# Optimization experiments

Measured on AMD Instinct MI355X. Metric: run time of the kernel, lower is better.

The kernel has to match this reference:

```python
import jax, jax.numpy as jnp
import numpy as np

N_NODES = 100000
N_EDGES = 1600000
D = 64


def setup_inputs() -> dict:
    key = jax.random.key(0)
    ks = jax.random.split(key, 9)
    x = jax.random.normal(ks[0], (N_NODES, D), dtype=jnp.float32)
    src = jax.random.randint(ks[1], (N_EDGES,), 0, N_NODES, dtype=jnp.int64)
    dst = jax.random.randint(ks[2], (N_EDGES,), 0, N_NODES, dtype=jnp.int64)
    s = 1.0 / np.sqrt(D)
    W_self1 = jax.random.normal(ks[3], (D, D), dtype=jnp.float32) * s
    W_neigh1 = jax.random.normal(ks[4], (D, D), dtype=jnp.float32) * s
    b1 = jnp.zeros((D,), dtype=jnp.float32)
    W_self2 = jax.random.normal(ks[5], (D, D), dtype=jnp.float32) * s
    W_neigh2 = jax.random.normal(ks[6], (D, D), dtype=jnp.float32) * s
    b2 = jnp.zeros((D,), dtype=jnp.float32)
    return {"x": x, "src": src, "dst": dst,
            "W_self1": W_self1, "W_neigh1": W_neigh1, "b1": b1,
            "W_self2": W_self2, "W_neigh2": W_neigh2, "b2": b2}


def _sage_layer(h, src, dst, W_self, W_neigh, b, n_nodes):
    # gather source-node features along edges: [E, d]
    msg = h[src]
    # sum messages into destination nodes, then normalize by in-degree (mean agg)
    agg = jax.ops.segment_sum(msg, dst, num_segments=n_nodes)
    deg = jax.ops.segment_sum(jnp.ones((src.shape[0], 1), h.dtype), dst,
                              num_segments=n_nodes)
    h_neigh = agg / jnp.maximum(deg, 1.0)
    # DGL SAGEConv (mean): fc_self(h) + fc_neigh(h_neigh) + bias
    return h @ W_self + h_neigh @ W_neigh + b


def reference(x, src, dst, W_self1, W_neigh1, b1, W_self2, W_neigh2, b2):
    n = x.shape[0]
    h = _sage_layer(x, src, dst, W_self1, W_neigh1, b1, n)
    # note: source module's forward applies no activation between layers
    h = _sage_layer(h, src, dst, W_self2, W_neigh2, b2, n)
    return h
```

## Files before the change

### kernel.cpp

```cpp
#include <hip/hip_runtime.h>
#include <hip/hip_bf16.h>


#define D 64
#define CAP 64
#define BNODES 256
#define BCAP 4736
#define MAXNB 512

typedef __bf16 bf16x8 __attribute__((ext_vector_type(8)));
typedef float  f32x4  __attribute__((ext_vector_type(4)));

__device__ __forceinline__ unsigned pack2(float a, float b) {
    __hip_bfloat162 t = __float22bfloat162_rn(make_float2(a, b));
    return *(unsigned*)&t;
}
__device__ __forceinline__ unsigned short f2b(float f) {
    __hip_bfloat16 b = __float2bfloat16(f);
    return *(unsigned short*)&b;
}


__global__ void __launch_bounds__(256)
cvt_kernel(const float4* __restrict__ x, uint4* __restrict__ y, int n8) {
    int i = blockIdx.x * blockDim.x + threadIdx.x;
    if (i < n8) {
        float4 a = x[2 * i], b = x[2 * i + 1];
        uint4 o;
        o.x = pack2(a.x, a.y);
        o.y = pack2(a.z, a.w);
        o.z = pack2(b.x, b.y);
        o.w = pack2(b.z, b.w);
        y[i] = o;
    }
}


__global__ void __launch_bounds__(64)
zrow_kernel(unsigned* __restrict__ a, unsigned* __restrict__ b) {
    int t = threadIdx.x;
    if (t < 32) a[t] = 0u;
    else        b[t - 32] = 0u;
}


__global__ void __launch_bounds__(256)
bin_kernel(const int* __restrict__ src, const int* __restrict__ dst,
           int* __restrict__ gcur, int* __restrict__ gbucket, int E, int NB) {
    __shared__ int hist[MAXNB];
    for (int i = threadIdx.x; i < NB; i += 256) hist[i] = 0;
    __syncthreads();

    const int t        = threadIdx.x;
    const int e4_total = E >> 2;
    const int base4    = blockIdx.x * 1024;

    int4 sv[4], dv[4];
    bool have[4];
    #pragma unroll
    for (int k = 0; k < 4; ++k) {
        int i4 = base4 + t + k * 256;
        have[k] = i4 < e4_total;
        if (have[k]) {
            sv[k] = ((const int4*)src)[i4];
            dv[k] = ((const int4*)dst)[i4];
        }
    }

    #pragma unroll
    for (int k = 0; k < 4; ++k) if (have[k]) {
        atomicAdd(&hist[dv[k].x >> 8], 1);
        atomicAdd(&hist[dv[k].y >> 8], 1);
        atomicAdd(&hist[dv[k].z >> 8], 1);
        atomicAdd(&hist[dv[k].w >> 8], 1);
    }

    int  tail_s = 0, tail_d = 0;
    bool have_tail = false;
    if (blockIdx.x == 0) {
        int e = (e4_total << 2) + t;
        if (e < E) {
            tail_s = src[e]; tail_d = dst[e]; have_tail = true;
            atomicAdd(&hist[tail_d >> 8], 1);
        }
    }
    __syncthreads();

    for (int i = threadIdx.x; i < NB; i += 256) {
        int c = hist[i];
        hist[i] = (c > 0) ? atomicAdd(&gcur[i], c) : 0;
    }
    __syncthreads();

    #pragma unroll
    for (int k = 0; k < 4; ++k) if (have[k]) {
        int4 s = sv[k], d = dv[k];
        int b, p;
        b = d.x >> 8; p = atomicAdd(&hist[b], 1); if (p < BCAP) gbucket[b * BCAP + p] = ((d.x & 255) << 17) | s.x;
        b = d.y >> 8; p = atomicAdd(&hist[b], 1); if (p < BCAP) gbucket[b * BCAP + p] = ((d.y & 255) << 17) | s.y;
        b = d.z >> 8; p = atomicAdd(&hist[b], 1); if (p < BCAP) gbucket[b * BCAP + p] = ((d.z & 255) << 17) | s.z;
        b = d.w >> 8; p = atomicAdd(&hist[b], 1); if (p < BCAP) gbucket[b * BCAP + p] = ((d.w & 255) << 17) | s.w;
    }
    if (have_tail) {
        int b = tail_d >> 8, p = atomicAdd(&hist[b], 1);
        if (p < BCAP) gbucket[b * BCAP + p] = ((tail_d & 255) << 17) | tail_s;
    }
}


__global__ void __launch_bounds__(256)
ellify_kernel(const int* __restrict__ gcur, const int* __restrict__ gbucket,
              int* __restrict__ cnt, int* __restrict__ edge_idx, int N) {
    __shared__ int scnt[BNODES];
    scnt[threadIdx.x] = 0;
    __syncthreads();

    const int b     = blockIdx.x;
    const int ne    = min(gcur[b], BCAP);
    const int node0 = b << 8;

    for (int e = threadIdx.x; e < ne; e += 256) {
        int p   = gbucket[b * BCAP + e];
        int s   = p & 0x1FFFF;
        int ld  = p >> 17;
        int pos = atomicAdd(&scnt[ld], 1);
        if (pos < CAP) edge_idx[(size_t)(node0 + ld) * CAP + pos] = s;
    }
    __syncthreads();

    int node = node0 + threadIdx.x;
    if (node < N) {
        int raw = scnt[threadIdx.x];
        cnt[node] = raw;
        int c  = min(raw, CAP);
        int c8 = (c + 7) & ~7;
        for (int p = c; p < c8; ++p)
            edge_idx[(size_t)node * CAP + p] = N;
    }
}


__device__ __forceinline__ void acc8(float& a0, float& a1, float& a2, float& a3,
                                     float& a4, float& a5, float& a6, float& a7,
                                     uint4 u) {
    a0 += __uint_as_float(u.x << 16);
    a1 += __uint_as_float(u.x & 0xffff0000u);
    a2 += __uint_as_float(u.y << 16);
    a3 += __uint_as_float(u.y & 0xffff0000u);
    a4 += __uint_as_float(u.z << 16);
    a5 += __uint_as_float(u.z & 0xffff0000u);
    a6 += __uint_as_float(u.w << 16);
    a7 += __uint_as_float(u.w & 0xffff0000u);
}

__global__ void __launch_bounds__(256, 4)
gather_kernel(const unsigned short* __restrict__ h,
              const int* __restrict__ cnt,
              const int* __restrict__ edge_idx,
              unsigned short* __restrict__ agg, int N) {
    const int lane = threadIdx.x & 63;
    const int q    = lane & 7;
    const int g    = lane >> 3;
    const int wave = blockIdx.x * (blockDim.x >> 6) + (threadIdx.x >> 6);
    const int node = wave * 8 + g;
    if (node >= N) return;

    const uint4* __restrict__ h4 = (const uint4*)h;

    const int count = min(cnt[node], CAP);
    const int c8    = (count + 7) & ~7;
    const int start = node * CAP;

    float a0 = 0.f, a1 = 0.f, a2 = 0.f, a3 = 0.f;
    float a4 = 0.f, a5 = 0.f, a6 = 0.f, a7 = 0.f;

    for (int j = 0; j < c8; j += 8) {
        const int sreg = edge_idx[start + j + q];
        const int b0 = g << 3;
        const int s0 = __shfl(sreg, b0 + 0, 64);
        const int s1 = __shfl(sreg, b0 + 1, 64);
        const int s2 = __shfl(sreg, b0 + 2, 64);
        const int s3 = __shfl(sreg, b0 + 3, 64);
        const int s4 = __shfl(sreg, b0 + 4, 64);
        const int s5 = __shfl(sreg, b0 + 5, 64);
        const int s6 = __shfl(sreg, b0 + 6, 64);
        const int s7 = __shfl(sreg, b0 + 7, 64);
        uint4 u0 = h4[(size_t)s0 * 8 + q];
        uint4 u1 = h4[(size_t)s1 * 8 + q];
        uint4 u2 = h4[(size_t)s2 * 8 + q];
        uint4 u3 = h4[(size_t)s3 * 8 + q];
        uint4 u4 = h4[(size_t)s4 * 8 + q];
        uint4 u5 = h4[(size_t)s5 * 8 + q];
        uint4 u6 = h4[(size_t)s6 * 8 + q];
        uint4 u7 = h4[(size_t)s7 * 8 + q];
        acc8(a0, a1, a2, a3, a4, a5, a6, a7, u0);
        acc8(a0, a1, a2, a3, a4, a5, a6, a7, u1);
        acc8(a0, a1, a2, a3, a4, a5, a6, a7, u2);
        acc8(a0, a1, a2, a3, a4, a5, a6, a7, u3);
        acc8(a0, a1, a2, a3, a4, a5, a6, a7, u4);
        acc8(a0, a1, a2, a3, a4, a5, a6, a7, u5);
        acc8(a0, a1, a2, a3, a4, a5, a6, a7, u6);
        acc8(a0, a1, a2, a3, a4, a5, a6, a7, u7);
    }

    const float inv = 1.0f / fmaxf((float)count, 1.0f);
    uint4 o;
    o.x = pack2(a0 * inv, a1 * inv);
    o.y = pack2(a2 * inv, a3 * inv);
    o.z = pack2(a4 * inv, a5 * inv);
    o.w = pack2(a6 * inv, a7 * inv);
    ((uint4*)agg)[node * 8 + q] = o;
}


__device__ __forceinline__ bf16x8 cvt8(float4 a, float4 b) {
    union { bf16x8 v; __hip_bfloat162 p[4]; } u;
    u.p[0] = __float22bfloat162_rn(make_float2(a.x, a.y));
    u.p[1] = __float22bfloat162_rn(make_float2(a.z, a.w));
    u.p[2] = __float22bfloat162_rn(make_float2(b.x, b.y));
    u.p[3] = __float22bfloat162_rn(make_float2(b.z, b.w));
    return u.v;
}
__device__ __forceinline__ bf16x8 asbf(uint4 u) {
    union { uint4 a; bf16x8 v; } c; c.a = u; return c.v;
}

__global__ void __launch_bounds__(256)
combine_kernel(const unsigned short* __restrict__ h,
               const unsigned short* __restrict__ agg,
               const float* __restrict__ Wself,
               const float* __restrict__ Wneigh,
               const float* __restrict__ bias,
               float* __restrict__ out_f32,
               unsigned short* __restrict__ out_bf16, int N) {
    const int lane = threadIdx.x & 63;
    const int col  = lane & 15;
    const int quad = lane >> 4;
    const int wave = blockIdx.x * (blockDim.x >> 6) + (threadIdx.x >> 6);
    const int n_waves = gridDim.x * (blockDim.x >> 6);

    bf16x8 Bf[4][4];
    #pragma unroll
    for (int nt = 0; nt < 4; ++nt) {
        const int n = nt * 16 + col;
        #pragma unroll
        for (int kk = 0; kk < 4; ++kk) {
            const float* W = (kk < 2) ? Wself : Wneigh;
            const int kbase = (kk & 1) * 32 + quad * 8;
            float w0 = W[(kbase + 0) * D + n];
            float w1 = W[(kbase + 1) * D + n];
            float w2 = W[(kbase + 2) * D + n];
            float w3 = W[(kbase + 3) * D + n];
            float w4 = W[(kbase + 4) * D + n];
            float w5 = W[(kbase + 5) * D + n];
            float w6 = W[(kbase + 6) * D + n];
            float w7 = W[(kbase + 7) * D + n];
            Bf[nt][kk] = cvt8(make_float4(w0, w1, w2, w3), make_float4(w4, w5, w6, w7));
        }
    }

    float bv[4];
    #pragma unroll
    for (int nt = 0; nt < 4; ++nt) bv[nt] = bias[nt * 16 + col];

    const uint4* __restrict__ h4 = (const uint4*)h;
    const uint4* __restrict__ a4 = (const uint4*)agg;

    const int tiles = (N + 15) >> 4;
    for (int t = wave; t < tiles; t += n_waves) {
        int row = t * 16 + col;
        if (row >= N) row = N - 1;

        bf16x8 A0 = asbf(h4[(size_t)row * 8 + quad]);
        bf16x8 A1 = asbf(h4[(size_t)row * 8 + 4 + quad]);
        bf16x8 A2 = asbf(a4[(size_t)row * 8 + quad]);
        bf16x8 A3 = asbf(a4[(size_t)row * 8 + 4 + quad]);

        #pragma unroll
        for (int nt = 0; nt < 4; ++nt) {
            f32x4 acc = {bv[nt], bv[nt], bv[nt], bv[nt]};
            acc = __builtin_amdgcn_mfma_f32_16x16x32_bf16(A0, Bf[nt][0], acc, 0, 0, 0);
            acc = __builtin_amdgcn_mfma_f32_16x16x32_bf16(A1, Bf[nt][1], acc, 0, 0, 0);
            acc = __builtin_amdgcn_mfma_f32_16x16x32_bf16(A2, Bf[nt][2], acc, 0, 0, 0);
            acc = __builtin_amdgcn_mfma_f32_16x16x32_bf16(A3, Bf[nt][3], acc, 0, 0, 0);
            if (out_f32) {
                #pragma unroll
                for (int r = 0; r < 4; ++r) {
                    const int orow = t * 16 + quad * 4 + r;
                    if (orow < N) out_f32[(size_t)orow * D + nt * 16 + col] = acc[r];
                }
            } else {
                #pragma unroll
                for (int r = 0; r < 4; ++r) {
                    const int orow = t * 16 + quad * 4 + r;
                    if (orow < N) out_bf16[(size_t)orow * D + nt * 16 + col] = f2b(acc[r]);
                }
            }
        }
    }
}


extern "C" void kernel_launch(void* const* d_in, const int* in_sizes, int n_in,
                              void* d_out, int out_size, void* d_ws, size_t ws_size,
                              hipStream_t stream) {
    const float* x   = (const float*)d_in[0];
    const int*   src = (const int*)d_in[1];
    const int*   dst = (const int*)d_in[2];
    const float* Ws1 = (const float*)d_in[3];
    const float* Wn1 = (const float*)d_in[4];
    const float* b1  = (const float*)d_in[5];
    const float* Ws2 = (const float*)d_in[6];
    const float* Wn2 = (const float*)d_in[7];
    const float* b2  = (const float*)d_in[8];

    const int N = in_sizes[0] / D;
    const int E = in_sizes[1];

    float* out = (float*)d_out;

    const int NB = (N + BNODES - 1) / BNODES;

    int* gcur      = (int*)d_ws;
    int* cnt       = gcur + 512;
    int* edge_idx  = cnt + N;
    unsigned short* xb   = (unsigned short*)(edge_idx + (size_t)N * CAP);
    unsigned short* h1b  = xb + (size_t)(N + 1) * D;
    unsigned short* aggb = h1b + (size_t)(N + 1) * D;
    int* gbucket   = (int*)aggb;

    const int n8 = N * D / 8;
    cvt_kernel<<<(n8 + 255) / 256, 256, 0, stream>>>((const float4*)x, (uint4*)xb, n8);
    zrow_kernel<<<1, 64, 0, stream>>>((unsigned*)(xb + (size_t)N * D),
                                      (unsigned*)(h1b + (size_t)N * D));

    const int e4_total   = E >> 2;
    const int bin_blocks = (e4_total + 1023) / 1024 > 0 ? (e4_total + 1023) / 1024 : 1;
    hipMemsetAsync(gcur, 0, 512 * sizeof(int), stream);
    bin_kernel<<<bin_blocks, 256, 0, stream>>>(src, dst, gcur, gbucket, E, NB);
    ellify_kernel<<<NB, 256, 0, stream>>>(gcur, gbucket, cnt, edge_idx, N);

    const int gather_blocks  = (N + 31) / 32;
    const int combine_blocks = 512;

    gather_kernel<<<gather_blocks, 256, 0, stream>>>(xb, cnt, edge_idx, aggb, N);
    combine_kernel<<<combine_blocks, 256, 0, stream>>>(xb, aggb, Ws1, Wn1, b1,
                                                       nullptr, h1b, N);
    gather_kernel<<<gather_blocks, 256, 0, stream>>>(h1b, cnt, edge_idx, aggb, N);
    combine_kernel<<<combine_blocks, 256, 0, stream>>>(h1b, aggb, Ws2, Wn2, b2,
                                                       out, nullptr, N);
}
```

Baseline: 212.2 us.

## Fuse neighbor gather into MFMA combine and merge prep kernels

Gather-mean aggregation now runs inside the combine kernel: each wave gathers 16 rows' neighbor sums in registers, moves them into MFMA A-operand layout with lane shuffles, then multiplies. This drops the aggregated bf16 intermediate buffer and its global write and read. The binning, bf16 conversion and sentinel-row zeroing kernels are merged into one launch to cut launch overhead. In exchange the fused kernel uses more registers (launch bounds 3), launches one wave per tile, and builds the weight fragments in every block.

Measured after the change: 207.8 us. 2.1% less time.

```diff
diff --git a/kernel.cpp b/kernel.cpp
--- a/kernel.cpp
+++ b/kernel.cpp
@@ -22,8 +22,77 @@
 
 
 __global__ void __launch_bounds__(256)
-cvt_kernel(const float4* __restrict__ x, uint4* __restrict__ y, int n8) {
-    int i = blockIdx.x * blockDim.x + threadIdx.x;
+prep_kernel(const float4* __restrict__ x, uint4* __restrict__ xb4,
+            unsigned* __restrict__ xsent, unsigned* __restrict__ h1sent,
+            const int* __restrict__ src, const int* __restrict__ dst,
+            int* __restrict__ gcur, int* __restrict__ gbucket,
+            int E, int NB, int n8, int bin_blocks) {
+    const int bid = blockIdx.x;
+    const int t   = threadIdx.x;
+
+    if (bid < bin_blocks) {
+        __shared__ int hist[MAXNB];
+        for (int i = t; i < NB; i += 256) hist[i] = 0;
+        __syncthreads();
+
+        const int e4_total = E >> 2;
+        const int base4    = bid * 1024;
+
+        int4 sv[4], dv[4];
+        bool have[4];
+        #pragma unroll
+        for (int k = 0; k < 4; ++k) {
+            int i4 = base4 + t + k * 256;
+            have[k] = i4 < e4_total;
+            if (have[k]) {
+                sv[k] = ((const int4*)src)[i4];
+                dv[k] = ((const int4*)dst)[i4];
+            }
+        }
+
+        #pragma unroll
+        for (int k = 0; k < 4; ++k) if (have[k]) {
+            atomicAdd(&hist[dv[k].x >> 8], 1);
+            atomicAdd(&hist[dv[k].y >> 8], 1);
+            atomicAdd(&hist[dv[k].z >> 8], 1);
+            atomicAdd(&hist[dv[k].w >> 8], 1);
+        }
+
+        int  tail_s = 0, tail_d = 0;
+        bool have_tail = false;
+        if (bid == 0) {
+            int e = (e4_total << 2) + t;
+            if (e < E) {
+                tail_s = src[e]; tail_d = dst[e]; have_tail = true;
+                atomicAdd(&hist[tail_d >> 8], 1);
+            }
+        }
+        __syncthreads();
+
+        for (int i = t; i < NB; i += 256) {
+            int c = hist[i];
+            hist[i] = (c > 0) ? atomicAdd(&gcur[i], c) : 0;
+        }
+        __syncthreads();
+
+        #pragma unroll
+        for (int k = 0; k < 4; ++k) if (have[k]) {
+            int4 s = sv[k], d = dv[k];
+            int b, p;
+            b = d.x >> 8; p = atomicAdd(&hist[b], 1); if (p < BCAP) gbucket[b * BCAP + p] = ((d.x & 255) << 17) | s.x;
+            b = d.y >> 8; p = atomicAdd(&hist[b], 1); if (p < BCAP) gbucket[b * BCAP + p] = ((d.y & 255) << 17) | s.y;
+            b = d.z >> 8; p = atomicAdd(&hist[b], 1); if (p < BCAP) gbucket[b * BCAP + p] = ((d.z & 255) << 17) | s.z;
+            b = d.w >> 8; p = atomicAdd(&hist[b], 1); if (p < BCAP) gbucket[b * BCAP + p] = ((d.w & 255) << 17) | s.w;
+        }
+        if (have_tail) {
+            int b = tail_d >> 8, p = atomicAdd(&hist[b], 1);
+            if (p < BCAP) gbucket[b * BCAP + p] = ((tail_d & 255) << 17) | tail_s;
+        }
+        return;
+    }
+
+    const int cb = bid - bin_blocks;
+    const int i  = cb * 256 + t;
     if (i < n8) {
         float4 a = x[2 * i], b = x[2 * i + 1];
         uint4 o;
@@ -31,79 +100,11 @@
         o.y = pack2(a.z, a.w);
         o.z = pack2(b.x, b.y);
         o.w = pack2(b.z, b.w);
-        y[i] = o;
-    }
-}
-
-
-__global__ void __launch_bounds__(64)
-zrow_kernel(unsigned* __restrict__ a, unsigned* __restrict__ b) {
-    int t = threadIdx.x;
-    if (t < 32) a[t] = 0u;
-    else        b[t - 32] = 0u;
-}
-
-
-__global__ void __launch_bounds__(256)
-bin_kernel(const int* __restrict__ src, const int* __restrict__ dst,
-           int* __restrict__ gcur, int* __restrict__ gbucket, int E, int NB) {
-    __shared__ int hist[MAXNB];
-    for (int i = threadIdx.x; i < NB; i += 256) hist[i] = 0;
-    __syncthreads();
-
-    const int t        = threadIdx.x;
-    const int e4_total = E >> 2;
-    const int base4    = blockIdx.x * 1024;
-
-    int4 sv[4], dv[4];
-    bool have[4];
-    #pragma unroll
-    for (int k = 0; k < 4; ++k) {
-        int i4 = base4 + t + k * 256;
-        have[k] = i4 < e4_total;
-        if (have[k]) {
-            sv[k] = ((const int4*)src)[i4];
-            dv[k] = ((const int4*)dst)[i4];
-        }
-    }
-
-    #pragma unroll
-    for (int k = 0; k < 4; ++k) if (have[k]) {
-        atomicAdd(&hist[dv[k].x >> 8], 1);
-        atomicAdd(&hist[dv[k].y >> 8], 1);
-        atomicAdd(&hist[dv[k].z >> 8], 1);
-        atomicAdd(&hist[dv[k].w >> 8], 1);
-    }
-
-    int  tail_s = 0, tail_d = 0;
-    bool have_tail = false;
-    if (blockIdx.x == 0) {
-        int e = (e4_total << 2) + t;
-        if (e < E) {
-            tail_s = src[e]; tail_d = dst[e]; have_tail = true;
-            atomicAdd(&hist[tail_d >> 8], 1);
-        }
-    }
-    __syncthreads();
-
-    for (int i = threadIdx.x; i < NB; i += 256) {
-        int c = hist[i];
-        hist[i] = (c > 0) ? atomicAdd(&gcur[i], c) : 0;
-    }
-    __syncthreads();
-
-    #pragma unroll
-    for (int k = 0; k < 4; ++k) if (have[k]) {
-        int4 s = sv[k], d = dv[k];
-        int b, p;
-        b = d.x >> 8; p = atomicAdd(&hist[b], 1); if (p < BCAP) gbucket[b * BCAP + p] = ((d.x & 255) << 17) | s.x;
-        b = d.y >> 8; p = atomicAdd(&hist[b], 1); if (p < BCAP) gbucket[b * BCAP + p] = ((d.y & 255) << 17) | s.y;
-        b = d.z >> 8; p = atomicAdd(&hist[b], 1); if (p < BCAP) gbucket[b * BCAP + p] = ((d.z & 255) << 17) | s.z;
-        b = d.w >> 8; p = atomicAdd(&hist[b], 1); if (p < BCAP) gbucket[b * BCAP + p] = ((d.w & 255) << 17) | s.w;
-    }
-    if (have_tail) {
-        int b = tail_d >> 8, p = atomicAdd(&hist[b], 1);
-        if (p < BCAP) gbucket[b * BCAP + p] = ((tail_d & 255) << 17) | tail_s;
+        xb4[i] = o;
+    }
+    if (cb == 0 && t < 64) {
+        if (t < 32) xsent[t] = 0u;
+        else        h1sent[t - 32] = 0u;
     }
 }
 
@@ -153,30 +154,20 @@
     a7 += __uint_as_float(u.w & 0xffff0000u);
 }
 
-__global__ void __launch_bounds__(256, 4)
-gather_kernel(const unsigned short* __restrict__ h,
-              const int* __restrict__ cnt,
-              const int* __restrict__ edge_idx,
-              unsigned short* __restrict__ agg, int N) {
-    const int lane = threadIdx.x & 63;
-    const int q    = lane & 7;
-    const int g    = lane >> 3;
-    const int wave = blockIdx.x * (blockDim.x >> 6) + (threadIdx.x >> 6);
-    const int node = wave * 8 + g;
-    if (node >= N) return;
-
-    const uint4* __restrict__ h4 = (const uint4*)h;
-
-    const int count = min(cnt[node], CAP);
+__device__ __forceinline__ uint4 gather_row8(const uint4* __restrict__ h4,
+                                             const int* __restrict__ cnt,
+                                             const int* __restrict__ edge_idx,
+                                             int node, int N, int q, int g) {
+    const int count = (node < N) ? min(cnt[node], CAP) : 0;
     const int c8    = (count + 7) & ~7;
     const int start = node * CAP;
+    const int b0    = g << 3;
 
     float a0 = 0.f, a1 = 0.f, a2 = 0.f, a3 = 0.f;
     float a4 = 0.f, a5 = 0.f, a6 = 0.f, a7 = 0.f;
 
     for (int j = 0; j < c8; j += 8) {
         const int sreg = edge_idx[start + j + q];
-        const int b0 = g << 3;
         const int s0 = __shfl(sreg, b0 + 0, 64);
         const int s1 = __shfl(sreg, b0 + 1, 64);
         const int s2 = __shfl(sreg, b0 + 2, 64);
@@ -209,9 +200,8 @@
     o.y = pack2(a2 * inv, a3 * inv);
     o.z = pack2(a4 * inv, a5 * inv);
     o.w = pack2(a6 * inv, a7 * inv);
-    ((uint4*)agg)[node * 8 + q] = o;
-}
-
+    return o;
+}
 
 __device__ __forceinline__ bf16x8 cvt8(float4 a, float4 b) {
     union { bf16x8 v; __hip_bfloat162 p[4]; } u;
@@ -225,15 +215,18 @@
     union { uint4 a; bf16x8 v; } c; c.a = u; return c.v;
 }
 
-__global__ void __launch_bounds__(256)
-combine_kernel(const unsigned short* __restrict__ h,
-               const unsigned short* __restrict__ agg,
-               const float* __restrict__ Wself,
-               const float* __restrict__ Wneigh,
-               const float* __restrict__ bias,
-               float* __restrict__ out_f32,
-               unsigned short* __restrict__ out_bf16, int N) {
+__global__ void __launch_bounds__(256, 3)
+fused_kernel(const unsigned short* __restrict__ h,
+             const int* __restrict__ cnt,
+             const int* __restrict__ edge_idx,
+             const float* __restrict__ Wself,
+             const float* __restrict__ Wneigh,
+             const float* __restrict__ bias,
+             float* __restrict__ out_f32,
+             unsigned short* __restrict__ out_bf16, int N) {
     const int lane = threadIdx.x & 63;
+    const int q    = lane & 7;
+    const int g    = lane >> 3;
     const int col  = lane & 15;
     const int quad = lane >> 4;
     const int wave = blockIdx.x * (blockDim.x >> 6) + (threadIdx.x >> 6);
@@ -264,17 +257,41 @@
     for (int nt = 0; nt < 4; ++nt) bv[nt] = bias[nt * 16 + col];
 
     const uint4* __restrict__ h4 = (const uint4*)h;
-    const uint4* __restrict__ a4 = (const uint4*)agg;
 
     const int tiles = (N + 15) >> 4;
     for (int t = wave; t < tiles; t += n_waves) {
+        uint4 P0 = gather_row8(h4, cnt, edge_idx, t * 16 + g,     N, q, g);
+
         int row = t * 16 + col;
         if (row >= N) row = N - 1;
-
-        bf16x8 A0 = asbf(h4[(size_t)row * 8 + quad]);
-        bf16x8 A1 = asbf(h4[(size_t)row * 8 + 4 + quad]);
-        bf16x8 A2 = asbf(a4[(size_t)row * 8 + quad]);
-        bf16x8 A3 = asbf(a4[(size_t)row * 8 + 4 + quad]);
+        uint4 A0u = h4[(size_t)row * 8 + quad];
+        uint4 A1u = h4[(size_t)row * 8 + 4 + quad];
+
+        uint4 P1 = gather_row8(h4, cnt, edge_idx, t * 16 + 8 + g, N, q, g);
+
+        const int srcA2 = ((lane & 7) << 3) + quad;
+        const int srcA3 = srcA2 + 4;
+        const bool hi   = (lane & 8) != 0;
+        uint4 A2u, A3u;
+        {
+            unsigned l0 = __shfl(P0.x, srcA2, 64), h0 = __shfl(P1.x, srcA2, 64);
+            unsigned l1 = __shfl(P0.y, srcA2, 64), h1 = __shfl(P1.y, srcA2, 64);
+            unsigned l2 = __shfl(P0.z, srcA2, 64), h2 = __shfl(P1.z, srcA2, 64);
+            unsigned l3 = __shfl(P0.w, srcA2, 64), h3 = __shfl(P1.w, srcA2, 64);
+            A2u.x = hi ? h0 : l0;  A2u.y = hi ? h1 : l1;
+            A2u.z = hi ? h2 : l2;  A2u.w = hi ? h3 : l3;
+        }
+        {
+            unsigned l0 = __shfl(P0.x, srcA3, 64), h0 = __shfl(P1.x, srcA3, 64);
+            unsigned l1 = __shfl(P0.y, srcA3, 64), h1 = __shfl(P1.y, srcA3, 64);
+            unsigned l2 = __shfl(P0.z, srcA3, 64), h2 = __shfl(P1.z, srcA3, 64);
+            unsigned l3 = __shfl(P0.w, srcA3, 64), h3 = __shfl(P1.w, srcA3, 64);
+            A3u.x = hi ? h0 : l0;  A3u.y = hi ? h1 : l1;
+            A3u.z = hi ? h2 : l2;  A3u.w = hi ? h3 : l3;
+        }
+
+        bf16x8 A0 = asbf(A0u), A1 = asbf(A1u);
+        bf16x8 A2 = asbf(A2u), A3 = asbf(A3u);
 
         #pragma unroll
         for (int nt = 0; nt < 4; ++nt) {
@@ -326,27 +343,27 @@
     int* edge_idx  = cnt + N;
     unsigned short* xb   = (unsigned short*)(edge_idx + (size_t)N * CAP);
     unsigned short* h1b  = xb + (size_t)(N + 1) * D;
-    unsigned short* aggb = h1b + (size_t)(N + 1) * D;
-    int* gbucket   = (int*)aggb;
-
-    const int n8 = N * D / 8;
-    cvt_kernel<<<(n8 + 255) / 256, 256, 0, stream>>>((const float4*)x, (uint4*)xb, n8);
-    zrow_kernel<<<1, 64, 0, stream>>>((unsigned*)(xb + (size_t)N * D),
-                                      (unsigned*)(h1b + (size_t)N * D));
-
+    int* gbucket   = (int*)(h1b + (size_t)(N + 1) * D);
+
+    const int n8         = N * D / 8;
+    const int cvt_blocks = (n8 + 255) / 256;
     const int e4_total   = E >> 2;
     const int bin_blocks = (e4_total + 1023) / 1024 > 0 ? (e4_total + 1023) / 1024 : 1;
+
     hipMemsetAsync(gcur, 0, 512 * sizeof(int), stream);
-    bin_kernel<<<bin_blocks, 256, 0, stream>>>(src, dst, gcur, gbucket, E, NB);
+
+    prep_kernel<<<bin_blocks + cvt_blocks, 256, 0, stream>>>(
+        (const float4*)x, (uint4*)xb,
+        (unsigned*)(xb + (size_t)N * D), (unsigned*)(h1b + (size_t)N * D),
+        src, dst, gcur, gbucket, E, NB, n8, bin_blocks);
+
     ellify_kernel<<<NB, 256, 0, stream>>>(gcur, gbucket, cnt, edge_idx, N);
 
-    const int gather_blocks  = (N + 31) / 32;
-    const int combine_blocks = 512;
-
-    gather_kernel<<<gather_blocks, 256, 0, stream>>>(xb, cnt, edge_idx, aggb, N);
-    combine_kernel<<<combine_blocks, 256, 0, stream>>>(xb, aggb, Ws1, Wn1, b1,
-                                                       nullptr, h1b, N);
-    gather_kernel<<<gather_blocks, 256, 0, stream>>>(h1b, cnt, edge_idx, aggb, N);
-    combine_kernel<<<combine_blocks, 256, 0, stream>>>(h1b, aggb, Ws2, Wn2, b2,
-                                                       out, nullptr, N);
-}
+    const int tiles  = (N + 15) / 16;
+    const int fblocks = (tiles + 3) / 4;
+
+    fused_kernel<<<fblocks, 256, 0, stream>>>(xb, cnt, edge_idx, Ws1, Wn1, b1,
+                                              nullptr, h1b, N);
+    fused_kernel<<<fblocks, 256, 0, stream>>>(h1b, cnt, edge_idx, Ws2, Wn2, b2,
+                                              out, nullptr, N);
+}
```
